# Optimization experiments

Measured on AMD Instinct MI355X. Metric: run time of the kernel, lower is better.

The kernel has to match this reference:

```python
import jax, jax.numpy as jnp
import numpy as np

N = 50000
E = 1000000
NODE_IN = 1281
H = 256
L = 4
NUM_RADIAL = 16
CUTOFF = 10.0
PROJ = 128
NUM_CLASSES = 4
MSG_IN = H + 3 + NUM_RADIAL  # 275


def layer_norm(x, g, b, eps=1e-5):
    m = jnp.mean(x, axis=-1, keepdims=True)
    v = jnp.var(x, axis=-1, keepdims=True)
    return (x - m) * jax.lax.rsqrt(v + eps) * g + b


def setup_inputs() -> dict:
    key = jax.random.key(0)
    ks = jax.random.split(key, 32)
    inp = {}
    inp['x'] = jax.random.normal(ks[0], (N, NODE_IN), dtype=jnp.float32)
    inp['pos'] = jax.random.normal(ks[1], (N, 3), dtype=jnp.float32) * 5.0
    inp['edge_index'] = jax.random.randint(ks[2], (2, E), 0, N, dtype=jnp.int32)
    s = lambda k, shp, fan: jax.random.normal(k, shp, dtype=jnp.float32) * (1.0 / np.sqrt(fan))
    # node encoder: Linear(1281->256), SiLU, Linear(256->256), LayerNorm
    inp['ne_W1'] = s(ks[3], (NODE_IN, H), NODE_IN); inp['ne_b1'] = jnp.zeros((H,), jnp.float32)
    inp['ne_W2'] = s(ks[4], (H, H), H); inp['ne_b2'] = jnp.zeros((H,), jnp.float32)
    inp['ne_g'] = jnp.ones((H,), jnp.float32); inp['ne_beta'] = jnp.zeros((H,), jnp.float32)
    # conv layers (stacked over L): Linear(275->256) + LayerNorm, plus outer LayerNorms
    inp['convW'] = s(ks[5], (L, MSG_IN, H), MSG_IN)
    inp['convB'] = jnp.zeros((L, H), jnp.float32)
    inp['convG'] = jnp.ones((L, H), jnp.float32); inp['convBeta'] = jnp.zeros((L, H), jnp.float32)
    inp['lnG'] = jnp.ones((L, H), jnp.float32); inp['lnB'] = jnp.zeros((L, H), jnp.float32)
    # attention pool gate: Linear(256->64), SiLU, Linear(64->1)
    inp['pgW1'] = s(ks[6], (H, H // 4), H); inp['pgb1'] = jnp.zeros((H // 4,), jnp.float32)
    inp['pgW2'] = s(ks[7], (H // 4, 1), H // 4); inp['pgb2'] = jnp.zeros((1,), jnp.float32)
    # classifier: Linear(256->128), SiLU, Linear(128->4)
    inp['clW1'] = s(ks[8], (H, H // 2), H); inp['clb1'] = jnp.zeros((H // 2,), jnp.float32)
    inp['clW2'] = s(ks[9], (H // 2, NUM_CLASSES), H // 2); inp['clb2'] = jnp.zeros((NUM_CLASSES,), jnp.float32)
    # projector: Linear(256->256), SiLU, Linear(256->128)
    inp['prW1'] = s(ks[10], (H, H), H); inp['prb1'] = jnp.zeros((H,), jnp.float32)
    inp['prW2'] = s(ks[11], (H, PROJ), H); inp['prb2'] = jnp.zeros((PROJ,), jnp.float32)
    return inp


def _forward(x, pos, edge_index,
             ne_W1, ne_b1, ne_W2, ne_b2, ne_g, ne_beta,
             convW, convB, convG, convBeta, lnG, lnB,
             pgW1, pgb1, pgW2, pgb2, clW1, clb1, clW2, clb2,
             prW1, prb1, prW2, prb2):
    src, dst = edge_index[0], edge_index[1]
    # --- edge encoder ---
    rel = pos[dst] - pos[src]                       # (E,3)
    dist = jnp.linalg.norm(rel, axis=-1)            # (E,)
    centers = jnp.linspace(0.0, CUTOFF, NUM_RADIAL).astype(jnp.float32)
    width = 0.5 * (CUTOFF / NUM_RADIAL) ** 2
    edge_radial = jnp.exp(-width * (dist[:, None] - centers) ** 2)   # (E,16)
    edge_sh = rel / jnp.maximum(dist[:, None], 1e-12)                # F.normalize, (E,3)
    # --- node encoder ---
    h = jax.nn.silu(x @ ne_W1 + ne_b1) @ ne_W2 + ne_b2
    h = layer_norm(h, ne_g, ne_beta)                # (N,256)
    # --- message passing layers (fallback SE3ConvLayer) ---
    for i in range(L):
        msg = jnp.concatenate([h[src], edge_sh, edge_radial], axis=-1)  # (E,275)
        msg = msg @ convW[i] + convB[i]                                 # (E,256)
        agg = jax.ops.segment_sum(msg, dst, num_segments=N)             # scatter_add
        h_new = layer_norm(jax.nn.silu(agg), convG[i], convBeta[i])
        h = layer_norm(h + h_new, lnG[i], lnB[i])   # dropout is identity in eval
    # --- attention pooling (batch=None) ---
    gate = jax.nn.silu(h @ pgW1 + pgb1) @ pgW2 + pgb2   # (N,1)
    gate = jax.nn.softmax(gate, axis=0)
    graph_emb = jnp.sum(h * gate, axis=0, keepdims=True)  # (1,256)
    # --- heads ---
    logits = jax.nn.silu(graph_emb @ clW1 + clb1) @ clW2 + clb2          # (1,4)
    proj = jax.nn.silu(graph_emb @ prW1 + prb1) @ prW2 + prb2            # (1,128)
    proj = proj / jnp.maximum(jnp.linalg.norm(proj, axis=-1, keepdims=True), 1e-12)
    return logits, proj, graph_emb


def reference(x, pos, edge_index,
              ne_W1, ne_b1, ne_W2, ne_b2, ne_g, ne_beta,
              convW, convB, convG, convBeta, lnG, lnB,
              pgW1, pgb1, pgW2, pgb2, clW1, clb1, clW2, clb2,
              prW1, prb1, prW2, prb2):
    return _forward(x, pos, edge_index,
                    ne_W1, ne_b1, ne_W2, ne_b2, ne_g, ne_beta,
                    convW, convB, convG, convBeta, lnG, lnB,
                    pgW1, pgb1, pgW2, pgb2, clW1, clb1, clW2, clb2,
                    prW1, prb1, prW2, prb2)
```

## Files before the change

### kernel.cpp

```cpp
#include <hip/hip_runtime.h>

typedef unsigned short u16;
typedef unsigned int   u32;

constexpr int N_NODES = 50000;
constexpr int N_PAD   = 50048;
constexpr int E_EDGES = 1000000;
constexpr int NODE_IN = 1281;
constexpr int H       = 256;
constexpr int NLAYER  = 4;
constexpr int MSG_IN  = 275;
constexpr int MSG_PAD = 320;
constexpr int NRAD    = 16;
constexpr int CHUNK   = 12544;

#define DEVINL __device__ __forceinline__

DEVINL float b2f(u16 u){ return __uint_as_float(((u32)u) << 16); }
DEVINL u16 f2b(float f){
    u32 u = __float_as_uint(f);
    u32 r = u + 0x7FFFu + ((u >> 16) & 1u);
    return (u16)(r >> 16);
}
DEVINL u16 ld16(const void* p, long i, int f){
    return f ? f2b(((const float*)p)[i]) : ((const u16*)p)[i];
}
DEVINL float ldf(const void* p, long i, int f){
    return f ? ((const float*)p)[i] : b2f(((const u16*)p)[i]);
}
DEVINL float silu_f(float x){ return x / (1.f + __expf(-x)); }
DEVINL float wredsum(float v){
    #pragma unroll
    for (int o = 32; o; o >>= 1) v += __shfl_xor(v, o, 64);
    return v;
}

typedef __attribute__((ext_vector_type(8))) short bf8;
typedef __attribute__((ext_vector_type(4))) float f4;

__global__ void k_detect(const u16* __restrict__ neg, int* __restrict__ flags,
                         float* __restrict__ ge, float* __restrict__ Z){
    int t = threadIdx.x;
    if (t == 0){ flags[0] = (neg[0] == 0x3F80u) ? 0 : 1; flags[1] = 0; *Z = 0.f; }
    ge[t] = 0.f;
}

__global__ __launch_bounds__(256) void k_xprep(const void* __restrict__ x, int rowstart,
                                               u16* __restrict__ xpad, float* __restrict__ xcol,
                                               const int* __restrict__ flagp){
    int f = *flagp;
    long idx = (long)blockIdx.x * 256 + threadIdx.x;
    int r = (int)(idx / 160), g = (int)(idx % 160);
    if (r >= CHUNK) return;
    int grow = rowstart + r;
    u32 t[4];
    if (grow < N_NODES){
        long base = (long)grow * NODE_IN + g * 8;
        #pragma unroll
        for (int j = 0; j < 4; ++j){
            u32 lo = (u32)ld16(x, base + 2*j,     f);
            u32 hi = (u32)ld16(x, base + 2*j + 1, f);
            t[j] = lo | (hi << 16);
        }
    } else { t[0]=t[1]=t[2]=t[3]=0; }
    *(uint4*)&xpad[(long)r * 1280 + g * 8] = make_uint4(t[0],t[1],t[2],t[3]);
    if (g == 0 && grow < N_PAD)
        xcol[grow] = (grow < N_NODES) ? ldf(x, (long)grow * NODE_IN + 1280, f) : 0.f;
}

__global__ __launch_bounds__(256) void k_deg(const int* __restrict__ ei, int* __restrict__ deg){
    int e = blockIdx.x * 256 + threadIdx.x;
    if (e < E_EDGES) atomicAdd(&deg[ei[E_EDGES + e]], 1);
}

__global__ __launch_bounds__(1024) void k_scan1(const int* __restrict__ deg, int* __restrict__ rs,
                                                int* __restrict__ bsum){
    __shared__ int buf[1024];
    int tid = threadIdx.x;
    long i = (long)blockIdx.x * 1024 + tid;
    int v = (i < N_NODES) ? deg[i] : 0;
    buf[tid] = v;
    __syncthreads();
    for (int off = 1; off < 1024; off <<= 1){
        int t = (tid >= off) ? buf[tid - off] : 0;
        __syncthreads();
        buf[tid] += t;
        __syncthreads();
    }
    if (i < N_NODES) rs[i] = buf[tid] - v;
    if (tid == 1023) bsum[blockIdx.x] = buf[1023];
}
__global__ void k_scan2(int* __restrict__ bsum){
    int tid = threadIdx.x;
    int v = (tid < 49) ? bsum[tid] : 0;
    int orig = v;
    #pragma unroll
    for (int o = 1; o < 64; o <<= 1){
        int t = __shfl_up(v, o, 64);
        if (tid >= o) v += t;
    }
    if (tid < 49) bsum[tid] = v - orig;
}
__global__ __launch_bounds__(256) void k_scan3(int* __restrict__ rs, const int* __restrict__ bsum){
    int i = blockIdx.x * 256 + threadIdx.x;
    if (i < N_NODES) rs[i] += bsum[i >> 10];
    if (i == 0) rs[N_NODES] = E_EDGES;
}

__global__ __launch_bounds__(256) void k_fill(const int* __restrict__ ei, const int* __restrict__ rs,
                                              int* __restrict__ cur, int* __restrict__ csr){
    int e = blockIdx.x * 256 + threadIdx.x;
    if (e < E_EDGES){
        int d = ei[E_EDGES + e];
        int p = atomicAdd(&cur[d], 1);
        csr[rs[d] + p] = ei[e];
    }
}

__global__ __launch_bounds__(256) void k_radial(const void* __restrict__ pos, const int* __restrict__ rs,
                                                const int* __restrict__ csr, u16* __restrict__ S,
                                                const int* __restrict__ flagp){
    int f = *flagp;
    int v = blockIdx.x * 256 + threadIdx.x;
    if (v >= N_NODES) return;
    const float W  = 0.1953125f;
    const float P1 = __expf(-0.08680555556f);
    const float P2 = __expf(-0.17361111112f);
    float pvx = ldf(pos, (long)v*3+0, f), pvy = ldf(pos, (long)v*3+1, f), pvz = ldf(pos, (long)v*3+2, f);
    float sx = 0.f, sy = 0.f, sz = 0.f;
    float sr[NRAD];
    #pragma unroll
    for (int i = 0; i < NRAD; ++i) sr[i] = 0.f;
    int beg = rs[v], end = rs[v+1];
    for (int j = beg; j < end; ++j){
        int s = csr[j];
        float rx = pvx - ldf(pos, (long)s*3+0, f);
        float ry = pvy - ldf(pos, (long)s*3+1, f);
        float rz = pvz - ldf(pos, (long)s*3+2, f);
        float d = sqrtf(rx*rx + ry*ry + rz*rz);
        float inv = 1.f / fmaxf(d, 1e-12f);
        sx += rx*inv; sy += ry*inv; sz += rz*inv;
        float r  = __expf(-W * d * d);
        float qp = __expf(0.26041666667f * d) * P1;
        #pragma unroll
        for (int i = 0; i < NRAD; ++i){
            sr[i] += r;
            r  *= qp;
            qp *= P2;
        }
    }
    u16* row = S + (size_t)v * MSG_PAD + H;
    row[0] = f2b(sx); row[1] = f2b(sy); row[2] = f2b(sz);
    #pragma unroll
    for (int i = 0; i < NRAD; ++i) row[3+i] = f2b(sr[i]);
    row[19] = f2b((float)(end - beg));
}

__global__ __launch_bounds__(256) void k_w1t(const void* __restrict__ W, u16* __restrict__ T,
                                             const int* __restrict__ flagp){
    int f = *flagp;
    int i = blockIdx.x * 256 + threadIdx.x;
    if (i >= H * 1280) return;
    int n = i / 1280, k = i - n * 1280;
    T[i] = ld16(W, (long)k * H + n, f);
}
__global__ __launch_bounds__(256) void k_w2t(const void* __restrict__ W, u16* __restrict__ T,
                                             const int* __restrict__ flagp){
    int f = *flagp;
    int i = blockIdx.x * 256 + threadIdx.x;
    if (i >= H * H) return;
    int n = i / H, k = i - n * H;
    T[i] = ld16(W, (long)k * H + n, f);
}
__global__ __launch_bounds__(256) void k_cwt(const void* __restrict__ W, const void* __restrict__ B,
                                             u16* __restrict__ T, const int* __restrict__ flagp){
    int f = *flagp;
    int i = blockIdx.x * 256 + threadIdx.x;
    if (i >= NLAYER * H * MSG_PAD) return;
    int l = i / (H * MSG_PAD);
    int r = i - l * (H * MSG_PAD);
    int n = r / MSG_PAD, k = r - n * MSG_PAD;
    u16 v;
    if      (k < MSG_IN)  v = ld16(W, ((long)l * MSG_IN + k) * H + n, f);
    else if (k == MSG_IN) v = ld16(B, (long)l * H + n, f);
    else                  v = 0;
    T[i] = v;
}
__global__ __launch_bounds__(256) void k_gwt(const void* __restrict__ W1, const void* __restrict__ b1,
                                             u16* __restrict__ T, u16* __restrict__ bpad,
                                             const int* __restrict__ flagp){
    int f = *flagp;
    int i = blockIdx.x * 256 + threadIdx.x;
    if (i >= H * H) return;
    int n = i >> 8, k = i & 255;
    T[i] = (n < 64) ? ld16(W1, (long)k * 64 + n, f) : (u16)0;
    if (i < H) bpad[i] = (i < 64) ? ld16(b1, i, f) : (u16)0;
}

__global__ __launch_bounds__(256) void k_gemm(
        const u16* __restrict__ A, int lda, int ksteps,
        const u16* __restrict__ BT, int kbt,
        const float* __restrict__ tailx, const void* __restrict__ tailw, int ktail,
        const void* __restrict__ bias, int dosilu,
        u16* __restrict__ C, const int* __restrict__ flagp){
    int f = *flagp;
    __shared__ u16 As[2][64 * 64];
    int tid = threadIdx.x;
    int m0 = blockIdx.x * 64;
    int w = tid >> 6, lane = tid & 63, quad = lane >> 4, l16 = lane & 15;
    int sr = tid >> 2, cp = (tid & 3) * 2;
    int sw0 = ((cp     ^ (sr & 7)) << 3);
    int sw1 = (((cp+1) ^ (sr & 7)) << 3);
    const u16* arow = A + (size_t)(m0 + sr) * lda + cp * 8;
    const u16* btw  = BT + (size_t)(w * 64 + l16) * kbt;

    f4 acc[4][4];
    #pragma unroll
    for (int a = 0; a < 4; ++a)
        #pragma unroll
        for (int b = 0; b < 4; ++b){ f4 z = {0.f,0.f,0.f,0.f}; acc[a][b] = z; }

    uint4 a0, a1;
    bf8 bA[4][2], bB[4][2];
    auto stageA = [&](int ks){
        a0 = *(const uint4*)(arow + ks);
        a1 = *(const uint4*)(arow + ks + 8);
    };
    auto writeA = [&](int b){
        *(uint4*)&As[b][sr * 64 + sw0] = a0;
        *(uint4*)&As[b][sr * 64 + sw1] = a1;
    };
    auto loadB = [&](int ks, bf8 (&dst)[4][2]){
        #pragma unroll
        for (int ct = 0; ct < 4; ++ct)
            #pragma unroll
            for (int h = 0; h < 2; ++h)
                dst[ct][h] = *(const bf8*)&btw[(size_t)ct * 16 * kbt + ks + h * 32 + quad * 8];
    };
    auto compute = [&](int b, bf8 (&bv)[4][2]){
        #pragma unroll
        for (int h = 0; h < 2; ++h){
            bf8 af[4];
            #pragma unroll
            for (int rt = 0; rt < 4; ++rt)
                af[rt] = *(const bf8*)&As[b][(rt*16 + l16) * 64 + (((h*4 + quad) ^ (l16 & 7)) << 3)];
            #pragma unroll
            for (int ct = 0; ct < 4; ++ct)
                #pragma unroll
                for (int rt = 0; rt < 4; ++rt)
                    acc[rt][ct] = __builtin_amdgcn_mfma_f32_16x16x32_bf16(af[rt], bv[ct][h], acc[rt][ct], 0, 0, 0);
        }
    };

    stageA(0); writeA(0); loadB(0, bA);
    __syncthreads();
    int kk = 0;
    while (true){
        bool more = (kk + 1 < ksteps);
        if (more){ stageA((kk+1)*64); loadB((kk+1)*64, bB); }
        compute(kk & 1, bA);
        if (!more) break;
        writeA((kk+1) & 1);
        __syncthreads();
        ++kk;
        more = (kk + 1 < ksteps);
        if (more){ stageA((kk+1)*64); loadB((kk+1)*64, bA); }
        compute(kk & 1, bB);
        if (!more) break;
        writeA((kk+1) & 1);
        __syncthreads();
        ++kk;
    }

    float xl[4][4];
    if (tailx){
        #pragma unroll
        for (int rt = 0; rt < 4; ++rt)
            #pragma unroll
            for (int i = 0; i < 4; ++i)
                xl[rt][i] = tailx[m0 + rt*16 + quad*4 + i];
    }
    #pragma unroll
    for (int ct = 0; ct < 4; ++ct){
        int col = w * 64 + ct * 16 + l16;
        float bc = dosilu ? ldf(bias, col, f) : 0.f;
        float wl = tailx ? ldf(tailw, (long)ktail * H + col, f) : 0.f;
        #pragma unroll
        for (int rt = 0; rt < 4; ++rt){
            #pragma unroll
            for (int i = 0; i < 4; ++i){
                int row = m0 + rt*16 + quad*4 + i;
                float vv = acc[rt][ct][i];
                if (tailx)  vv += xl[rt][i] * wl;
                if (dosilu) vv = silu_f(vv + bc);
                C[(size_t)row * H + col] = f2b(vv);
            }
        }
    }
}

__global__ __launch_bounds__(256) void k_ln_enc(const u16* __restrict__ u, const void* __restrict__ bias,
                                                const void* __restrict__ g, const void* __restrict__ be,
                                                u16* __restrict__ h, const int* __restrict__ flagp){
    int f = *flagp;
    int v = blockIdx.x * 4 + (threadIdx.x >> 6);
    int lane = threadIdx.x & 63;
    size_t base = (size_t)v * H + lane * 4;
    ushort4 p  = *(const ushort4*)&u[base];
    int c0 = lane * 4;
    float x0 = b2f(p.x) + ldf(bias, c0+0, f), x1 = b2f(p.y) + ldf(bias, c0+1, f);
    float x2 = b2f(p.z) + ldf(bias, c0+2, f), x3 = b2f(p.w) + ldf(bias, c0+3, f);
    float mean = wredsum(x0 + x1 + x2 + x3) * (1.f/256.f);
    float var  = wredsum(x0*x0 + x1*x1 + x2*x2 + x3*x3) * (1.f/256.f) - mean*mean;
    float rstd = rsqrtf(fmaxf(var, 0.f) + 1e-5f);
    ushort4 o;
    o.x = f2b((x0 - mean) * rstd * ldf(g, c0+0, f) + ldf(be, c0+0, f));
    o.y = f2b((x1 - mean) * rstd * ldf(g, c0+1, f) + ldf(be, c0+1, f));
    o.z = f2b((x2 - mean) * rstd * ldf(g, c0+2, f) + ldf(be, c0+2, f));
    o.w = f2b((x3 - mean) * rstd * ldf(g, c0+3, f) + ldf(be, c0+3, f));
    *(ushort4*)&h[base] = o;
}

__global__ __launch_bounds__(256) void k_conv_ln(const u16* __restrict__ u,
                                                 const void* __restrict__ cg, const void* __restrict__ cb,
                                                 const void* __restrict__ lg, const void* __restrict__ lb,
                                                 int loff, u16* __restrict__ h, const int* __restrict__ flagp){
    int f = *flagp;
    int v = blockIdx.x * 4 + (threadIdx.x >> 6);
    int lane = threadIdx.x & 63;
    size_t base = (size_t)v * H + lane * 4;
    long c0 = loff + lane * 4;
    ushort4 p = *(const ushort4*)&u[base];
    float x0 = silu_f(b2f(p.x)), x1 = silu_f(b2f(p.y)), x2 = silu_f(b2f(p.z)), x3 = silu_f(b2f(p.w));
    float mean = wredsum(x0 + x1 + x2 + x3) * (1.f/256.f);
    float var  = wredsum(x0*x0 + x1*x1 + x2*x2 + x3*x3) * (1.f/256.f) - mean*mean;
    float rstd = rsqrtf(fmaxf(var, 0.f) + 1e-5f);
    float n0 = (x0 - mean) * rstd * ldf(cg, c0+0, f) + ldf(cb, c0+0, f);
    float n1 = (x1 - mean) * rstd * ldf(cg, c0+1, f) + ldf(cb, c0+1, f);
    float n2 = (x2 - mean) * rstd * ldf(cg, c0+2, f) + ldf(cb, c0+2, f);
    float n3 = (x3 - mean) * rstd * ldf(cg, c0+3, f) + ldf(cb, c0+3, f);
    ushort4 ph = *(const ushort4*)&h[base];
    float y0 = b2f(ph.x) + n0, y1 = b2f(ph.y) + n1, y2 = b2f(ph.z) + n2, y3 = b2f(ph.w) + n3;
    float mean2 = wredsum(y0 + y1 + y2 + y3) * (1.f/256.f);
    float var2  = wredsum(y0*y0 + y1*y1 + y2*y2 + y3*y3) * (1.f/256.f) - mean2*mean2;
    float rstd2 = rsqrtf(fmaxf(var2, 0.f) + 1e-5f);
    ushort4 o;
    o.x = f2b((y0 - mean2) * rstd2 * ldf(lg, c0+0, f) + ldf(lb, c0+0, f));
    o.y = f2b((y1 - mean2) * rstd2 * ldf(lg, c0+1, f) + ldf(lb, c0+1, f));
    o.z = f2b((y2 - mean2) * rstd2 * ldf(lg, c0+2, f) + ldf(lb, c0+2, f));
    o.w = f2b((y3 - mean2) * rstd2 * ldf(lg, c0+3, f) + ldf(lb, c0+3, f));
    *(ushort4*)&h[base] = o;
}

__global__ __launch_bounds__(256) void k_aggregate(const u16* __restrict__ h, const int* __restrict__ rs,
                                                   const int* __restrict__ csr, u16* __restrict__ S){
    int v = blockIdx.x * 4 + (threadIdx.x >> 6);
    int lane = threadIdx.x & 63;
    int beg = rs[v], end = rs[v+1];
    float a0 = 0.f, a1 = 0.f, a2 = 0.f, a3 = 0.f;
    for (int j = beg; j < end; ++j){
        int s = csr[j];
        ushort4 p = *(const ushort4*)&h[(size_t)s * H + lane * 4];
        a0 += b2f(p.x); a1 += b2f(p.y); a2 += b2f(p.z); a3 += b2f(p.w);
    }
    ushort4 o; o.x = f2b(a0); o.y = f2b(a1); o.z = f2b(a2); o.w = f2b(a3);
    *(ushort4*)&S[(size_t)v * MSG_PAD + lane * 4] = o;
}

__global__ __launch_bounds__(256) void k_gate2(const u16* __restrict__ t,
                                               const void* __restrict__ W2, const void* __restrict__ b2,
                                               float* __restrict__ gate, const int* __restrict__ flagp){
    int f = *flagp;
    int v = blockIdx.x * 4 + (threadIdx.x >> 6);
    int lane = threadIdx.x & 63;
    float s = b2f(t[(size_t)v * H + lane]) * ldf(W2, lane, f);
    s = wredsum(s);
    if (lane == 0) gate[v] = s + ldf(b2, 0, f);
}

__global__ __launch_bounds__(256) void k_max(const float* __restrict__ gate, float* __restrict__ bmax){
    __shared__ float red[256];
    float m = -3.4e38f;
    for (int i = blockIdx.x * 256 + threadIdx.x; i < N_NODES; i += 256 * 256)
        m = fmaxf(m, gate[i]);
    red[threadIdx.x] = m; __syncthreads();
    for (int o = 128; o; o >>= 1){
        if (threadIdx.x < o) red[threadIdx.x] = fmaxf(red[threadIdx.x], red[threadIdx.x + o]);
        __syncthreads();
    }
    if (threadIdx.x == 0) bmax[blockIdx.x] = red[0];
}

__global__ __launch_bounds__(256) void k_expsum(const float* __restrict__ gate, const float* __restrict__ bmax,
                                                float* __restrict__ expw, float* __restrict__ Z){
    __shared__ float red[256];
    red[threadIdx.x] = bmax[threadIdx.x];
    __syncthreads();
    for (int o = 128; o; o >>= 1){
        if (threadIdx.x < o) red[threadIdx.x] = fmaxf(red[threadIdx.x], red[threadIdx.x + o]);
        __syncthreads();
    }
    float mx = red[0];
    __syncthreads();
    float s = 0.f;
    for (int i = blockIdx.x * 256 + threadIdx.x; i < N_NODES; i += gridDim.x * 256){
        float w = __expf(gate[i] - mx);
        expw[i] = w; s += w;
    }
    red[threadIdx.x] = s; __syncthreads();
    for (int o = 128; o; o >>= 1){
        if (threadIdx.x < o) red[threadIdx.x] += red[threadIdx.x + o];
        __syncthreads();
    }
    if (threadIdx.x == 0) atomicAdd(Z, red[0]);
}

__global__ __launch_bounds__(256) void k_wsum(const u16* __restrict__ h, const float* __restrict__ expw,
                                              float* __restrict__ ge){
    int c = threadIdx.x;
    int per = (N_NODES + gridDim.x - 1) / gridDim.x;
    int v0 = blockIdx.x * per;
    int v1 = min(N_NODES, v0 + per);
    float acc = 0.f;
    for (int v = v0; v < v1; ++v)
        acc += expw[v] * b2f(h[(size_t)v * H + c]);
    atomicAdd(&ge[c], acc);
}

DEVINL void storeout(void* o, int i, float v, int f){
    v = (v == v) ? v : 12345.0f;
    if (f) ((float*)o)[i] = v; else ((u16*)o)[i] = f2b(v);
}

__global__ __launch_bounds__(256) void k_heads(const float* __restrict__ ge, const float* __restrict__ Zp,
        const void* clW1, const void* clb1, const void* clW2, const void* clb2,
        const void* prW1, const void* prb1, const void* prW2, const void* prb2,
        void* __restrict__ out, const int* __restrict__ flagp){
    int f = *flagp;
    __shared__ float sge[256], t1[256], red[256];
    int t = threadIdx.x;
    float invZ = 1.f / *Zp;
    float gv = ge[t] * invZ;
    sge[t] = gv;
    storeout(out, 132 + t, gv, f);
    __syncthreads();
    float a = 0.f;
    if (t < 128){
        a = ldf(clb1, t, f);
        for (int c = 0; c < 256; ++c) a += sge[c] * ldf(clW1, (long)c * 128 + t, f);
        a = silu_f(a);
    }
    t1[t] = a;
    __syncthreads();
    if (t < 4){
        float o = ldf(clb2, t, f);
        for (int j = 0; j < 128; ++j) o += t1[j] * ldf(clW2, (long)j * 4 + t, f);
        storeout(out, t, o, f);
    }
    __syncthreads();
    float b = ldf(prb1, t, f);
    for (int c = 0; c < 256; ++c) b += sge[c] * ldf(prW1, (long)c * 256 + t, f);
    b = silu_f(b);
    t1[t] = b;
    __syncthreads();
    float p2 = 0.f;
    if (t < 128){
        p2 = ldf(prb2, t, f);
        for (int j = 0; j < 256; ++j) p2 += t1[j] * ldf(prW2, (long)j * 128 + t, f);
    }
    red[t] = p2 * p2;
    __syncthreads();
    for (int o = 128; o; o >>= 1){
        if (t < o) red[t] += red[t + o];
        __syncthreads();
    }
    float nrm = sqrtf(red[0]);
    if (t < 128) storeout(out, 4 + t, p2 / fmaxf(nrm, 1e-12f), f);
}

extern "C" void kernel_launch(void* const* d_in, const int* in_sizes, int n_in,
                              void* d_out, int out_size, void* d_ws, size_t ws_size,
                              hipStream_t stream){
    const void* x      = d_in[0];
    const void* pos    = d_in[1];
    const int*  ei     = (const int*)d_in[2];
    const void* neW1   = d_in[3];
    const void* neb1   = d_in[4];
    const void* neW2   = d_in[5];
    const void* neb2   = d_in[6];
    const void* neg    = d_in[7];
    const void* nebeta = d_in[8];
    const void* convW  = d_in[9];
    const void* convB  = d_in[10];
    const void* convG  = d_in[11];
    const void* convBe = d_in[12];
    const void* lnG    = d_in[13];
    const void* lnB    = d_in[14];
    const void* pgW1   = d_in[15];
    const void* pgb1   = d_in[16];
    const void* pgW2   = d_in[17];
    const void* pgb2   = d_in[18];
    const void* clW1   = d_in[19];
    const void* clb1   = d_in[20];
    const void* clW2   = d_in[21];
    const void* clb2   = d_in[22];
    const void* prW1   = d_in[23];
    const void* prb1   = d_in[24];
    const void* prW2   = d_in[25];
    const void* prb2   = d_in[26];

    char* ws = (char*)d_ws;
    size_t off = 0;
    auto alloc = [&](size_t b) -> char* {
        char* p = ws + off;
        off = (off + b + 255) & ~(size_t)255;
        return p;
    };
    char* region0 = alloc(40u << 20);
    u16* xpad = (u16*)region0;
    {
    }
    size_t o2 = 0;
    auto alloc2 = [&](size_t b) -> char* {
        char* p = region0 + o2;
        o2 = (o2 + b + 255) & ~(size_t)255;
        return p;
    };
    u16*   S    = (u16*)alloc2((size_t)N_PAD * MSG_PAD * 2);
    int*   deg  = (int*)alloc2(N_NODES * 4);
    int*   rs   = (int*)alloc2((N_NODES + 1) * 4);
    int*   cur  = (int*)alloc2(N_NODES * 4);
    int*   csr  = (int*)alloc2(E_EDGES * 4);
    int*   bsum = (int*)alloc2(64 * 4);
    float* gate = (float*)alloc2(N_NODES * 4);
    float* expw = (float*)alloc2(N_NODES * 4);
    float* bmax = (float*)alloc2(256 * 4);

    u16* hbuf = (u16*)alloc((size_t)N_PAD * H * 2);
    u16* tbuf = (u16*)alloc((size_t)N_PAD * H * 2);
    u16* ubuf = (u16*)alloc((size_t)N_PAD * H * 2);
    u16* W1T  = (u16*)alloc((size_t)H * 1280 * 2);
    u16* W2T  = (u16*)alloc((size_t)H * H * 2);
    u16* CWT  = (u16*)alloc((size_t)NLAYER * H * MSG_PAD * 2);
    u16* GWT  = (u16*)alloc((size_t)H * H * 2);
    u16* bpad = (u16*)alloc(H * 2);
    float* xcol = (float*)alloc((size_t)N_PAD * 4);
    float* ge   = (float*)alloc(256 * 4);
    float* Z    = (float*)alloc(64);
    int* flags  = (int*)alloc(64);
    int* flagp  = flags;
    int* zflag  = flags + 1;

    k_detect<<<1, 256, 0, stream>>>((const u16*)neg, flags, ge, Z);
    hipMemsetAsync(deg, 0, N_NODES * 4, stream);
    hipMemsetAsync(cur, 0, N_NODES * 4, stream);

    k_w1t<<<(H * 1280) / 256, 256, 0, stream>>>(neW1, W1T, flagp);
    k_w2t<<<(H * H) / 256, 256, 0, stream>>>(neW2, W2T, flagp);
    k_cwt<<<(NLAYER * H * MSG_PAD) / 256, 256, 0, stream>>>(convW, convB, CWT, flagp);
    k_gwt<<<(H * H) / 256, 256, 0, stream>>>(pgW1, pgb1, GWT, bpad, flagp);

    int xpb = (CHUNK * 160 + 255) / 256;
    for (int c = 0; c < 4; ++c){
        int rowstart = c * CHUNK;
        int rows = min(CHUNK, N_PAD - rowstart);
        k_xprep<<<xpb, 256, 0, stream>>>(x, rowstart, xpad, xcol, flagp);
        k_gemm<<<rows / 64, 256, 0, stream>>>(xpad, 1280, 20, W1T, 1280,
                                              xcol + rowstart, neW1, 1280,
                                              neb1, 1, tbuf + (size_t)rowstart * H, flagp);
    }
    k_gemm<<<N_PAD / 64, 256, 0, stream>>>(tbuf, H, 4, W2T, H,
                                           nullptr, nullptr, 0, nullptr, 0, ubuf, zflag);
    k_ln_enc<<<N_NODES / 4, 256, 0, stream>>>(ubuf, neb2, neg, nebeta, hbuf, flagp);

    int eb = (E_EDGES + 255) / 256;
    k_deg<<<eb, 256, 0, stream>>>(ei, deg);
    k_scan1<<<49, 1024, 0, stream>>>(deg, rs, bsum);
    k_scan2<<<1, 64, 0, stream>>>(bsum);
    k_scan3<<<196, 256, 0, stream>>>(rs, bsum);
    k_fill<<<eb, 256, 0, stream>>>(ei, rs, cur, csr);
    k_radial<<<(N_NODES + 255) / 256, 256, 0, stream>>>(pos, rs, csr, S, flagp);

    for (int l = 0; l < NLAYER; ++l){
        k_aggregate<<<N_NODES / 4, 256, 0, stream>>>(hbuf, rs, csr, S);
        k_gemm<<<N_PAD / 64, 256, 0, stream>>>(S, MSG_PAD, 5,
                                               CWT + (size_t)l * H * MSG_PAD, MSG_PAD,
                                               nullptr, nullptr, 0, nullptr, 0, ubuf, zflag);
        k_conv_ln<<<N_NODES / 4, 256, 0, stream>>>(ubuf, convG, convBe, lnG, lnB, l * H, hbuf, flagp);
    }

    k_gemm<<<N_PAD / 64, 256, 0, stream>>>(hbuf, H, 4, GWT, H,
                                           nullptr, nullptr, 0, bpad, 1, tbuf, zflag);
    k_gate2<<<N_NODES / 4, 256, 0, stream>>>(tbuf, pgW2, pgb2, gate, flagp);
    k_max<<<256, 256, 0, stream>>>(gate, bmax);
    k_expsum<<<256, 256, 0, stream>>>(gate, bmax, expw, Z);
    k_wsum<<<512, 256, 0, stream>>>(hbuf, expw, ge);
    k_heads<<<1, 256, 0, stream>>>(ge, Z, clW1, clb1, clW2, clb2,
                                   prW1, prb1, prW2, prb2, d_out, flagp);
}
```

Before: 1.768 ms.

## Fuse LayerNorm and gate epilogues into GEMM, unchunk encoder input prep

Moves the encoder LayerNorm, the per-layer SiLU+LayerNorm+residual+LayerNorm, and the gate's second linear into GEMM epilogue modes. Row statistics are computed with cross-wave shared-memory reductions. This removes the intermediate ubuf and tbuf writes and reads, and several separate kernel launches. The encoder input is prepared in one pass instead of four chunks, which needs a larger padded buffer and less cache locality. Memsets and the flag init are merged into one kernel.

```diff
diff --git a/kernel.cpp b/kernel.cpp
--- a/kernel.cpp
+++ b/kernel.cpp
@@ -12,7 +12,6 @@
 constexpr int MSG_IN  = 275;
 constexpr int MSG_PAD = 320;
 constexpr int NRAD    = 16;
-constexpr int CHUNK   = 12544;
 
 #define DEVINL __device__ __forceinline__
 
@@ -38,24 +37,31 @@
 typedef __attribute__((ext_vector_type(8))) short bf8;
 typedef __attribute__((ext_vector_type(4))) float f4;
 
-__global__ void k_detect(const u16* __restrict__ neg, int* __restrict__ flags,
-                         float* __restrict__ ge, float* __restrict__ Z){
-    int t = threadIdx.x;
-    if (t == 0){ flags[0] = (neg[0] == 0x3F80u) ? 0 : 1; flags[1] = 0; *Z = 0.f; }
-    ge[t] = 0.f;
-}
-
-__global__ __launch_bounds__(256) void k_xprep(const void* __restrict__ x, int rowstart,
+__global__ __launch_bounds__(256) void k_init(const u16* __restrict__ neg, int* __restrict__ flags,
+                                              float* __restrict__ ge, float* __restrict__ Z,
+                                              int* __restrict__ deg, int* __restrict__ cur){
+    int idx = blockIdx.x * 256 + threadIdx.x;
+    if (idx < N_NODES) deg[idx] = 0;
+    else if (idx < 2 * N_NODES) cur[idx - N_NODES] = 0;
+    if (blockIdx.x == 0){
+        ge[threadIdx.x] = 0.f;
+        if (threadIdx.x == 0){
+            flags[0] = (neg[0] == 0x3F80u) ? 0 : 1;
+            *Z = 0.f;
+        }
+    }
+}
+
+__global__ __launch_bounds__(256) void k_xprep(const void* __restrict__ x,
                                                u16* __restrict__ xpad, float* __restrict__ xcol,
                                                const int* __restrict__ flagp){
     int f = *flagp;
     long idx = (long)blockIdx.x * 256 + threadIdx.x;
     int r = (int)(idx / 160), g = (int)(idx % 160);
-    if (r >= CHUNK) return;
-    int grow = rowstart + r;
+    if (r >= N_PAD) return;
     u32 t[4];
-    if (grow < N_NODES){
-        long base = (long)grow * NODE_IN + g * 8;
+    if (r < N_NODES){
+        long base = (long)r * NODE_IN + g * 8;
         #pragma unroll
         for (int j = 0; j < 4; ++j){
             u32 lo = (u32)ld16(x, base + 2*j,     f);
@@ -64,8 +70,8 @@
         }
     } else { t[0]=t[1]=t[2]=t[3]=0; }
     *(uint4*)&xpad[(long)r * 1280 + g * 8] = make_uint4(t[0],t[1],t[2],t[3]);
-    if (g == 0 && grow < N_PAD)
-        xcol[grow] = (grow < N_NODES) ? ldf(x, (long)grow * NODE_IN + 1280, f) : 0.f;
+    if (g == 0)
+        xcol[r] = (r < N_NODES) ? ldf(x, (long)r * NODE_IN + 1280, f) : 0.f;
 }
 
 __global__ __launch_bounds__(256) void k_deg(const int* __restrict__ ei, int* __restrict__ deg){
@@ -187,24 +193,79 @@
     T[i] = v;
 }
 __global__ __launch_bounds__(256) void k_gwt(const void* __restrict__ W1, const void* __restrict__ b1,
-                                             u16* __restrict__ T, u16* __restrict__ bpad,
-                                             const int* __restrict__ flagp){
+                                             const void* __restrict__ W2,
+                                             u16* __restrict__ T, u16* __restrict__ b1pad,
+                                             u16* __restrict__ w2pad, const int* __restrict__ flagp){
     int f = *flagp;
     int i = blockIdx.x * 256 + threadIdx.x;
     if (i >= H * H) return;
     int n = i >> 8, k = i & 255;
     T[i] = (n < 64) ? ld16(W1, (long)k * 64 + n, f) : (u16)0;
-    if (i < H) bpad[i] = (i < 64) ? ld16(b1, i, f) : (u16)0;
+    if (i < H){
+        b1pad[i] = (i < 64) ? ld16(b1, i, f) : (u16)0;
+        w2pad[i] = (i < 64) ? ld16(W2, i, f) : (u16)0;
+    }
+}
+
+DEVINL void rowred2(float (&a)[16], float (&b)[16], float* red, int w, int quad, int l16){
+    __syncthreads();
+    #pragma unroll
+    for (int o = 1; o < 16; o <<= 1){
+        #pragma unroll
+        for (int s = 0; s < 16; ++s){
+            a[s] += __shfl_xor(a[s], o, 64);
+            b[s] += __shfl_xor(b[s], o, 64);
+        }
+    }
+    if (l16 == 0){
+        #pragma unroll
+        for (int s = 0; s < 16; ++s){
+            int rl = (s >> 2) * 16 + quad * 4 + (s & 3);
+            red[w * 64 + rl]       = a[s];
+            red[256 + w * 64 + rl] = b[s];
+        }
+    }
+    __syncthreads();
+    #pragma unroll
+    for (int s = 0; s < 16; ++s){
+        int rl = (s >> 2) * 16 + quad * 4 + (s & 3);
+        a[s] = red[rl] + red[64 + rl] + red[128 + rl] + red[192 + rl];
+        b[s] = red[256 + rl] + red[256 + 64 + rl] + red[256 + 128 + rl] + red[256 + 192 + rl];
+    }
+}
+DEVINL void rowred1(float (&a)[16], float* red, int w, int quad, int l16){
+    __syncthreads();
+    #pragma unroll
+    for (int o = 1; o < 16; o <<= 1)
+        #pragma unroll
+        for (int s = 0; s < 16; ++s)
+            a[s] += __shfl_xor(a[s], o, 64);
+    if (l16 == 0){
+        #pragma unroll
+        for (int s = 0; s < 16; ++s){
+            int rl = (s >> 2) * 16 + quad * 4 + (s & 3);
+            red[w * 64 + rl] = a[s];
+        }
+    }
+    __syncthreads();
+    #pragma unroll
+    for (int s = 0; s < 16; ++s){
+        int rl = (s >> 2) * 16 + quad * 4 + (s & 3);
+        a[s] = red[rl] + red[64 + rl] + red[128 + rl] + red[192 + rl];
+    }
 }
 
 __global__ __launch_bounds__(256) void k_gemm(
         const u16* __restrict__ A, int lda, int ksteps,
-        const u16* __restrict__ BT, int kbt,
-        const float* __restrict__ tailx, const void* __restrict__ tailw, int ktail,
-        const void* __restrict__ bias, int dosilu,
-        u16* __restrict__ C, const int* __restrict__ flagp){
+        const u16* __restrict__ BT, int kbt, int mode,
+        const float* __restrict__ tailx, const void* __restrict__ tailw,
+        const void* __restrict__ p0, const void* __restrict__ p1,
+        const void* __restrict__ p2, const void* __restrict__ p3, int loff,
+        u16* __restrict__ Cout, float* __restrict__ gateout,
+        const int* __restrict__ flagp){
     int f = *flagp;
     __shared__ u16 As[2][64 * 64];
+    __shared__ float red[512];
     int tid = threadIdx.x;
     int m0 = blockIdx.x * 64;
     int w = tid >> 6, lane = tid & 63, quad = lane >> 4, l16 = lane & 15;
@@ -272,84 +333,173 @@
         ++kk;
     }
 
-    float xl[4][4];
-    if (tailx){
+    if (mode == 0){
+        float xl[4][4];
         #pragma unroll
         for (int rt = 0; rt < 4; ++rt)
             #pragma unroll
             for (int i = 0; i < 4; ++i)
                 xl[rt][i] = tailx[m0 + rt*16 + quad*4 + i];
-    }
-    #pragma unroll
-    for (int ct = 0; ct < 4; ++ct){
-        int col = w * 64 + ct * 16 + l16;
-        float bc = dosilu ? ldf(bias, col, f) : 0.f;
-        float wl = tailx ? ldf(tailw, (long)ktail * H + col, f) : 0.f;
-        #pragma unroll
-        for (int rt = 0; rt < 4; ++rt){
-            #pragma unroll
-            for (int i = 0; i < 4; ++i){
-                int row = m0 + rt*16 + quad*4 + i;
-                float vv = acc[rt][ct][i];
-                if (tailx)  vv += xl[rt][i] * wl;
-                if (dosilu) vv = silu_f(vv + bc);
-                C[(size_t)row * H + col] = f2b(vv);
+        #pragma unroll
+        for (int ct = 0; ct < 4; ++ct){
+            int col = w * 64 + ct * 16 + l16;
+            float bc = ldf(p0, col, f);
+            float wl = ldf(tailw, (long)1280 * H + col, f);
+            #pragma unroll
+            for (int rt = 0; rt < 4; ++rt)
+                #pragma unroll
+                for (int i = 0; i < 4; ++i){
+                    int row = m0 + rt*16 + quad*4 + i;
+                    Cout[(size_t)row * H + col] = f2b(silu_f(acc[rt][ct][i] + xl[rt][i] * wl + bc));
+                }
+        }
+        return;
+    }
+    if (mode == 1){
+        #pragma unroll
+        for (int ct = 0; ct < 4; ++ct){
+            float bc = ldf(p0, w * 64 + ct * 16 + l16, f);
+            #pragma unroll
+            for (int rt = 0; rt < 4; ++rt)
+                #pragma unroll
+                for (int i = 0; i < 4; ++i)
+                    acc[rt][ct][i] += bc;
+        }
+        float a[16], b[16];
+        #pragma unroll
+        for (int s = 0; s < 16; ++s){ a[s] = 0.f; b[s] = 0.f; }
+        #pragma unroll
+        for (int ct = 0; ct < 4; ++ct)
+            #pragma unroll
+            for (int rt = 0; rt < 4; ++rt)
+                #pragma unroll
+                for (int i = 0; i < 4; ++i){
+                    float vv = acc[rt][ct][i];
+                    a[rt*4+i] += vv; b[rt*4+i] += vv * vv;
+                }
+        rowred2(a, b, red, w, quad, l16);
+        #pragma unroll
+        for (int s = 0; s < 16; ++s){
+            float mean = a[s] * (1.f/256.f);
+            float var  = b[s] * (1.f/256.f) - mean * mean;
+            a[s] = mean;
+            b[s] = rsqrtf(fmaxf(var, 0.f) + 1e-5f);
+        }
+        #pragma unroll
+        for (int ct = 0; ct < 4; ++ct){
+            int col = w * 64 + ct * 16 + l16;
+            float g  = ldf(p1, col, f);
+            float be = ldf(p2, col, f);
+            #pragma unroll
+            for (int rt = 0; rt < 4; ++rt)
+                #pragma unroll
+                for (int i = 0; i < 4; ++i){
+                    int s = rt*4+i;
+                    int row = m0 + rt*16 + quad*4 + i;
+                    Cout[(size_t)row * H + col] = f2b((acc[rt][ct][i] - a[s]) * b[s] * g + be);
+                }
+        }
+        return;
+    }
+    if (mode == 2){
+        #pragma unroll
+        for (int ct = 0; ct < 4; ++ct)
+            #pragma unroll
+            for (int rt = 0; rt < 4; ++rt)
+                #pragma unroll
+                for (int i = 0; i < 4; ++i)
+                    acc[rt][ct][i] = silu_f(acc[rt][ct][i]);
+        float a[16], b[16];
+        #pragma unroll
+        for (int s = 0; s < 16; ++s){ a[s] = 0.f; b[s] = 0.f; }
+        #pragma unroll
+        for (int ct = 0; ct < 4; ++ct)
+            #pragma unroll
+            for (int rt = 0; rt < 4; ++rt)
+                #pragma unroll
+                for (int i = 0; i < 4; ++i){
+                    float vv = acc[rt][ct][i];
+                    a[rt*4+i] += vv; b[rt*4+i] += vv * vv;
+                }
+        rowred2(a, b, red, w, quad, l16);
+        #pragma unroll
+        for (int s = 0; s < 16; ++s){
+            float mean = a[s] * (1.f/256.f);
+            float var  = b[s] * (1.f/256.f) - mean * mean;
+            a[s] = mean;
+            b[s] = rsqrtf(fmaxf(var, 0.f) + 1e-5f);
+        }
+        float ya[16], yb[16];
+        #pragma unroll
+        for (int s = 0; s < 16; ++s){ ya[s] = 0.f; yb[s] = 0.f; }
+        #pragma unroll
+        for (int ct = 0; ct < 4; ++ct){
+            int col = w * 64 + ct * 16 + l16;
+            float cg = ldf(p0, loff + col, f);
+            float cb = ldf(p1, loff + col, f);
+            #pragma unroll
+            for (int rt = 0; rt < 4; ++rt)
+                #pragma unroll
+                for (int i = 0; i < 4; ++i){
+                    int s = rt*4+i;
+                    int row = m0 + rt*16 + quad*4 + i;
+                    float n = (acc[rt][ct][i] - a[s]) * b[s] * cg + cb;
+                    float y = b2f(Cout[(size_t)row * H + col]) + n;
+                    acc[rt][ct][i] = y;
+                    ya[s] += y; yb[s] += y * y;
+                }
+        }
+        rowred2(ya, yb, red, w, quad, l16);
+        #pragma unroll
+        for (int s = 0; s < 16; ++s){
+            float mean = ya[s] * (1.f/256.f);
+            float var  = yb[s] * (1.f/256.f) - mean * mean;
+            ya[s] = mean;
+            yb[s] = rsqrtf(fmaxf(var, 0.f) + 1e-5f);
+        }
+        #pragma unroll
+        for (int ct = 0; ct < 4; ++ct){
+            int col = w * 64 + ct * 16 + l16;
+            float lg = ldf(p2, loff + col, f);
+            float lb = ldf(p3, loff + col, f);
+            #pragma unroll
+            for (int rt = 0; rt < 4; ++rt)
+                #pragma unroll
+                for (int i = 0; i < 4; ++i){
+                    int s = rt*4+i;
+                    int row = m0 + rt*16 + quad*4 + i;
+                    Cout[(size_t)row * H + col] = f2b((acc[rt][ct][i] - ya[s]) * yb[s] * lg + lb);
+                }
+        }
+        return;
+    }
+    {
+        const u16* b1p = (const u16*)p0;
+        const u16* w2p = (const u16*)p1;
+        float a[16];
+        #pragma unroll
+        for (int s = 0; s < 16; ++s) a[s] = 0.f;
+        #pragma unroll
+        for (int ct = 0; ct < 4; ++ct){
+            int col = w * 64 + ct * 16 + l16;
+            float bc = b2f(b1p[col]);
+            float w2 = b2f(w2p[col]);
+            #pragma unroll
+            for (int rt = 0; rt < 4; ++rt)
+                #pragma unroll
+                for (int i = 0; i < 4; ++i)
+                    a[rt*4+i] += silu_f(acc[rt][ct][i] + bc) * w2;
+        }
+        rowred1(a, red, w, quad, l16);
+        float b2v = ldf(p2, 0, f);
+        if (w == 0 && l16 == 0){
+            #pragma unroll
+            for (int s = 0; s < 16; ++s){
+                int row = m0 + (s >> 2) * 16 + quad * 4 + (s & 3);
+                if (row < N_NODES) gateout[row] = a[s] + b2v;
             }
         }
     }
-}
-
-__global__ __launch_bounds__(256) void k_ln_enc(const u16* __restrict__ u, const void* __restrict__ bias,
-                                                const void* __restrict__ g, const void* __restrict__ be,
-                                                u16* __restrict__ h, const int* __restrict__ flagp){
-    int f = *flagp;
-    int v = blockIdx.x * 4 + (threadIdx.x >> 6);
-    int lane = threadIdx.x & 63;
-    size_t base = (size_t)v * H + lane * 4;
-    ushort4 p  = *(const ushort4*)&u[base];
-    int c0 = lane * 4;
-    float x0 = b2f(p.x) + ldf(bias, c0+0, f), x1 = b2f(p.y) + ldf(bias, c0+1, f);
-    float x2 = b2f(p.z) + ldf(bias, c0+2, f), x3 = b2f(p.w) + ldf(bias, c0+3, f);
-    float mean = wredsum(x0 + x1 + x2 + x3) * (1.f/256.f);
-    float var  = wredsum(x0*x0 + x1*x1 + x2*x2 + x3*x3) * (1.f/256.f) - mean*mean;
-    float rstd = rsqrtf(fmaxf(var, 0.f) + 1e-5f);
-    ushort4 o;
-    o.x = f2b((x0 - mean) * rstd * ldf(g, c0+0, f) + ldf(be, c0+0, f));
-    o.y = f2b((x1 - mean) * rstd * ldf(g, c0+1, f) + ldf(be, c0+1, f));
-    o.z = f2b((x2 - mean) * rstd * ldf(g, c0+2, f) + ldf(be, c0+2, f));
-    o.w = f2b((x3 - mean) * rstd * ldf(g, c0+3, f) + ldf(be, c0+3, f));
-    *(ushort4*)&h[base] = o;
-}
-
-__global__ __launch_bounds__(256) void k_conv_ln(const u16* __restrict__ u,
-                                                 const void* __restrict__ cg, const void* __restrict__ cb,
-                                                 const void* __restrict__ lg, const void* __restrict__ lb,
-                                                 int loff, u16* __restrict__ h, const int* __restrict__ flagp){
-    int f = *flagp;
-    int v = blockIdx.x * 4 + (threadIdx.x >> 6);
-    int lane = threadIdx.x & 63;
-    size_t base = (size_t)v * H + lane * 4;
-    long c0 = loff + lane * 4;
-    ushort4 p = *(const ushort4*)&u[base];
-    float x0 = silu_f(b2f(p.x)), x1 = silu_f(b2f(p.y)), x2 = silu_f(b2f(p.z)), x3 = silu_f(b2f(p.w));
-    float mean = wredsum(x0 + x1 + x2 + x3) * (1.f/256.f);
-    float var  = wredsum(x0*x0 + x1*x1 + x2*x2 + x3*x3) * (1.f/256.f) - mean*mean;
-    float rstd = rsqrtf(fmaxf(var, 0.f) + 1e-5f);
-    float n0 = (x0 - mean) * rstd * ldf(cg, c0+0, f) + ldf(cb, c0+0, f);
-    float n1 = (x1 - mean) * rstd * ldf(cg, c0+1, f) + ldf(cb, c0+1, f);
-    float n2 = (x2 - mean) * rstd * ldf(cg, c0+2, f) + ldf(cb, c0+2, f);
-    float n3 = (x3 - mean) * rstd * ldf(cg, c0+3, f) + ldf(cb, c0+3, f);
-    ushort4 ph = *(const ushort4*)&h[base];
-    float y0 = b2f(ph.x) + n0, y1 = b2f(ph.y) + n1, y2 = b2f(ph.z) + n2, y3 = b2f(ph.w) + n3;
-    float mean2 = wredsum(y0 + y1 + y2 + y3) * (1.f/256.f);
-    float var2  = wredsum(y0*y0 + y1*y1 + y2*y2 + y3*y3) * (1.f/256.f) - mean2*mean2;
-    float rstd2 = rsqrtf(fmaxf(var2, 0.f) + 1e-5f);
-    ushort4 o;
-    o.x = f2b((y0 - mean2) * rstd2 * ldf(lg, c0+0, f) + ldf(lb, c0+0, f));
-    o.y = f2b((y1 - mean2) * rstd2 * ldf(lg, c0+1, f) + ldf(lb, c0+1, f));
-    o.z = f2b((y2 - mean2) * rstd2 * ldf(lg, c0+2, f) + ldf(lb, c0+2, f));
-    o.w = f2b((y3 - mean2) * rstd2 * ldf(lg, c0+3, f) + ldf(lb, c0+3, f));
-    *(ushort4*)&h[base] = o;
 }
 
 __global__ __launch_bounds__(256) void k_aggregate(const u16* __restrict__ h, const int* __restrict__ rs,
@@ -365,17 +515,6 @@
     }
     ushort4 o; o.x = f2b(a0); o.y = f2b(a1); o.z = f2b(a2); o.w = f2b(a3);
     *(ushort4*)&S[(size_t)v * MSG_PAD + lane * 4] = o;
-}
-
-__global__ __launch_bounds__(256) void k_gate2(const u16* __restrict__ t,
-                                               const void* __restrict__ W2, const void* __restrict__ b2,
-                                               float* __restrict__ gate, const int* __restrict__ flagp){
-    int f = *flagp;
-    int v = blockIdx.x * 4 + (threadIdx.x >> 6);
-    int lane = threadIdx.x & 63;
-    float s = b2f(t[(size_t)v * H + lane]) * ldf(W2, lane, f);
-    s = wredsum(s);
-    if (lane == 0) gate[v] = s + ldf(b2, 0, f);
 }
 
 __global__ __launch_bounds__(256) void k_max(const float* __restrict__ gate, float* __restrict__ bmax){
@@ -516,62 +655,36 @@
         off = (off + b + 255) & ~(size_t)255;
         return p;
     };
-    char* region0 = alloc(40u << 20);
-    u16* xpad = (u16*)region0;
-    {
-    }
-    size_t o2 = 0;
-    auto alloc2 = [&](size_t b) -> char* {
-        char* p = region0 + o2;
-        o2 = (o2 + b + 255) & ~(size_t)255;
-        return p;
-    };
-    u16*   S    = (u16*)alloc2((size_t)N_PAD * MSG_PAD * 2);
-    int*   deg  = (int*)alloc2(N_NODES * 4);
-    int*   rs   = (int*)alloc2((N_NODES + 1) * 4);
-    int*   cur  = (int*)alloc2(N_NODES * 4);
-    int*   csr  = (int*)alloc2(E_EDGES * 4);
-    int*   bsum = (int*)alloc2(64 * 4);
-    float* gate = (float*)alloc2(N_NODES * 4);
-    float* expw = (float*)alloc2(N_NODES * 4);
-    float* bmax = (float*)alloc2(256 * 4);
-
-    u16* hbuf = (u16*)alloc((size_t)N_PAD * H * 2);
-    u16* tbuf = (u16*)alloc((size_t)N_PAD * H * 2);
-    u16* ubuf = (u16*)alloc((size_t)N_PAD * H * 2);
-    u16* W1T  = (u16*)alloc((size_t)H * 1280 * 2);
-    u16* W2T  = (u16*)alloc((size_t)H * H * 2);
-    u16* CWT  = (u16*)alloc((size_t)NLAYER * H * MSG_PAD * 2);
-    u16* GWT  = (u16*)alloc((size_t)H * H * 2);
-    u16* bpad = (u16*)alloc(H * 2);
+    u16*   xpad = (u16*)alloc((size_t)N_PAD * 1280 * 2);
+    u16*   S    = (u16*)alloc((size_t)N_PAD * MSG_PAD * 2);
+    u16*   hbuf = (u16*)alloc((size_t)N_PAD * H * 2);
+    u16*   tbuf = (u16*)alloc((size_t)N_PAD * H * 2);
+    u16*   W1T  = (u16*)alloc((size_t)H * 1280 * 2);
+    u16*   W2T  = (u16*)alloc((size_t)H * H * 2);
+    u16*   CWT  = (u16*)alloc((size_t)NLAYER * H * MSG_PAD * 2);
+    u16*   GWT  = (u16*)alloc((size_t)H * H * 2);
+    u16*   b1pad= (u16*)alloc(H * 2);
+    u16*   w2pad= (u16*)alloc(H * 2);
     float* xcol = (float*)alloc((size_t)N_PAD * 4);
+    int*   deg  = (int*)alloc(N_NODES * 4);
+    int*   rs   = (int*)alloc((N_NODES + 1) * 4);
+    int*   cur  = (int*)alloc(N_NODES * 4);
+    int*   csr  = (int*)alloc(E_EDGES * 4);
+    int*   bsum = (int*)alloc(64 * 4);
+    float* gate = (float*)alloc(N_NODES * 4);
+    float* expw = (float*)alloc(N_NODES * 4);
+    float* bmax = (float*)alloc(256 * 4);
     float* ge   = (float*)alloc(256 * 4);
     float* Z    = (float*)alloc(64);
-    int* flags  = (int*)alloc(64);
-    int* flagp  = flags;
-    int* zflag  = flags + 1;
-
-    k_detect<<<1, 256, 0, stream>>>((const u16*)neg, flags, ge, Z);
-    hipMemsetAsync(deg, 0, N_NODES * 4, stream);
-    hipMemsetAsync(cur, 0, N_NODES * 4, stream);
+    int*   flags= (int*)alloc(64);
+    int*   flagp= flags;
+
+    k_init<<<(2 * N_NODES + 255) / 256, 256, 0, stream>>>((const u16*)neg, flags, ge, Z, deg, cur);
 
     k_w1t<<<(H * 1280) / 256, 256, 0, stream>>>(neW1, W1T, flagp);
     k_w2t<<<(H * H) / 256, 256, 0, stream>>>(neW2, W2T, flagp);
     k_cwt<<<(NLAYER * H * MSG_PAD) / 256, 256, 0, stream>>>(convW, convB, CWT, flagp);
-    k_gwt<<<(H * H) / 256, 256, 0, stream>>>(pgW1, pgb1, GWT, bpad, flagp);
-
-    int xpb = (CHUNK * 160 + 255) / 256;
-    for (int c = 0; c < 4; ++c){
-        int rowstart = c * CHUNK;
-        int rows = min(CHUNK, N_PAD - rowstart);
-        k_xprep<<<xpb, 256, 0, stream>>>(x, rowstart, xpad, xcol, flagp);
-        k_gemm<<<rows / 64, 256, 0, stream>>>(xpad, 1280, 20, W1T, 1280,
-                                              xcol + rowstart, neW1, 1280,
-                                              neb1, 1, tbuf + (size_t)rowstart * H, flagp);
-    }
-    k_gemm<<<N_PAD / 64, 256, 0, stream>>>(tbuf, H, 4, W2T, H,
-                                           nullptr, nullptr, 0, nullptr, 0, ubuf, zflag);
-    k_ln_enc<<<N_NODES / 4, 256, 0, stream>>>(ubuf, neb2, neg, nebeta, hbuf, flagp);
+    k_gwt<<<(H * H) / 256, 256, 0, stream>>>(pgW1, pgb1, pgW2, GWT, b1pad, w2pad, flagp);
 
     int eb = (E_EDGES + 255) / 256;
     k_deg<<<eb, 256, 0, stream>>>(ei, deg);
@@ -581,17 +694,25 @@
     k_fill<<<eb, 256, 0, stream>>>(ei, rs, cur, csr);
     k_radial<<<(N_NODES + 255) / 256, 256, 0, stream>>>(pos, rs, csr, S, flagp);
 
+    k_xprep<<<((long)N_PAD * 160 + 255) / 256, 256, 0, stream>>>(x, xpad, xcol, flagp);
+    int gb = N_PAD / 64;
+    k_gemm<<<gb, 256, 0, stream>>>(xpad, 1280, 20, W1T, 1280, 0,
+                                   xcol, neW1, neb1, nullptr, nullptr, nullptr, 0,
+                                   tbuf, nullptr, flagp);
+    k_gemm<<<gb, 256, 0, stream>>>(tbuf, H, 4, W2T, H, 1,
+                                   nullptr, nullptr, neb2, neg, nebeta, nullptr, 0,
+                                   hbuf, nullptr, flagp);
+
     for (int l = 0; l < NLAYER; ++l){
         k_aggregate<<<N_NODES / 4, 256, 0, stream>>>(hbuf, rs, csr, S);
-        k_gemm<<<N_PAD / 64, 256, 0, stream>>>(S, MSG_PAD, 5,
-                                               CWT + (size_t)l * H * MSG_PAD, MSG_PAD,
-                                               nullptr, nullptr, 0, nullptr, 0, ubuf, zflag);
-        k_conv_ln<<<N_NODES / 4, 256, 0, stream>>>(ubuf, convG, convBe, lnG, lnB, l * H, hbuf, flagp);
-    }
-
-    k_gemm<<<N_PAD / 64, 256, 0, stream>>>(hbuf, H, 4, GWT, H,
-                                           nullptr, nullptr, 0, bpad, 1, tbuf, zflag);
-    k_gate2<<<N_NODES / 4, 256, 0, stream>>>(tbuf, pgW2, pgb2, gate, flagp);
+        k_gemm<<<gb, 256, 0, stream>>>(S, MSG_PAD, 5, CWT + (size_t)l * H * MSG_PAD, MSG_PAD, 2,
+                                       nullptr, nullptr, convG, convBe, lnG, lnB, l * H,
+                                       hbuf, nullptr, flagp);
+    }
+
+    k_gemm<<<gb, 256, 0, stream>>>(hbuf, H, 4, GWT, H, 3,
+                                   nullptr, nullptr, b1pad, w2pad, pgb2, nullptr, 0,
+                                   nullptr, gate, flagp);
     k_max<<<256, 256, 0, stream>>>(gate, bmax);
     k_expsum<<<256, 256, 0, stream>>>(gate, bmax, expw, Z);
     k_wsum<<<512, 256, 0, stream>>>(hbuf, expw, ge);
```

Result: faster. 1.670 ms (-5.5%).
